# Performance work log

Hardware: AMD Instinct MI355X
Metric: run time of the kernel (lower is better)

Reference implementation:

```python
import jax, jax.numpy as jnp
import numpy as np

B, L, S, H, E = 2, 2048, 2048, 16, 64
EPS = 1e-8


def setup_inputs() -> dict:
    key = jax.random.key(0)
    k1, k2, k3, k4, k5 = jax.random.split(key, 5)
    query = jax.random.normal(k1, (B, L, H, E), dtype=jnp.float32)
    key_t = jax.random.normal(k2, (B, S, H, E), dtype=jnp.float32)
    value = jax.random.normal(k3, (B, S, H, E), dtype=jnp.float32)
    mask_miss_k = jax.random.randint(k4, (B, S, 1), 0, 2).astype(bool)
    mask_miss_q = jax.random.randint(k5, (B, L, 1), 0, 2).astype(bool)
    # monotone per-batch positions -> standard causal structure
    pos = jnp.broadcast_to(jnp.arange(L, dtype=jnp.int32)[None, :, None], (B, L, 1))
    return {"query": query, "key": key_t, "value": value,
            "mask_miss_k": mask_miss_k, "mask_miss_q": mask_miss_q,
            "pos": pos, "causal_mask": 1}


def reference(query, key, value, mask_miss_k, mask_miss_q, pos, causal_mask):
    # query: (B,L,H,E); key/value: (B,S,H,E)
    E_ = query.shape[-1]
    scale = 1.0 / np.sqrt(E_)
    scores = jnp.einsum('blhe,bshe->bhls', query, key)  # (B,H,L,S)
    if causal_mask:
        p = pos[..., 0]  # (B,L)
        causal_add = jnp.where(p[:, None, :] > p[:, :, None],
                               -jnp.inf, 0.0).astype(scores.dtype)  # (B,L,S)
        scores = scores + causal_add[:, None, :, :]
    # additive -inf masks for missing keys / queries
    m_k = jnp.where(mask_miss_k[..., 0][:, None, None, :], -jnp.inf, 0.0).astype(scores.dtype)
    m_q = jnp.where(mask_miss_q[..., 0][:, None, :, None], -jnp.inf, 0.0).astype(scores.dtype)
    # NOTE: scale multiplies (scores + M_k) exactly as in the original
    att = jnp.maximum(jax.nn.softmax(scale * (scores + m_k), axis=-1) + m_q, 0.0)
    # entropy of (post-relu, possibly unnormalized) attention weights
    entropy = -jnp.sum(att * jnp.log(jnp.clip(att, EPS, None)), axis=-1)  # (B,H,L)
    entropy = jnp.nan_to_num(entropy, nan=0.0)
    A = jnp.nan_to_num(att)  # dropout p=0 -> identity, then nan_to_num
    V = jnp.einsum('bhls,bshd->blhd', A, value)  # (B,L,H,E)
    return V, A, entropy
```

## Files before the change

kernel.cpp:

```cpp
#include <hip/hip_runtime.h>

#define BB 2
#define LL 2048
#define SS 2048
#define HH 16
#define EE 64
#define HE (HH*EE)
#define TS 64
#define SCALEF 0.125f
#define NEGBIG (-1e30f)

typedef __bf16 bf8 __attribute__((ext_vector_type(8)));
typedef float f4v __attribute__((ext_vector_type(4)));
typedef unsigned int u32;
typedef unsigned short u16;

#define V_ELEMS  ((size_t)BB*LL*HH*EE)
#define A_BASE   (V_ELEMS)
#define ENT_BASE (A_BASE + (size_t)BB*HH*LL*SS)

__device__ __forceinline__ u16 bfb(float f) {
    u32 u = __builtin_bit_cast(u32, f);
    return (u16)((u + 0x7fffu + ((u >> 16) & 1u)) >> 16);
}
__device__ __forceinline__ int swz8(int r) { return (((r) & 7) ^ (((r) >> 3) & 7)) << 4; }

__device__ __forceinline__ f4v mfma16(bf8 a, bf8 b, f4v c) {
    return __builtin_amdgcn_mfma_f32_16x16x32_bf16(a, b, c, 0, 0, 0);
}
__device__ __forceinline__ int maskv(const void* p, int i, int isB) {
    return isB ? (int)((const unsigned char*)p)[i] : ((const int*)p)[i];
}
__device__ __forceinline__ void barrier_lds() {
    asm volatile("s_waitcnt lgkmcnt(0)" ::: "memory");
    __builtin_amdgcn_s_barrier();
    asm volatile("" ::: "memory");
}
__device__ __forceinline__ uint4 pack8(float4 f0, float4 f1) {
    uint4 wv;
    wv.x = bfb(f0.x) | ((u32)bfb(f0.y) << 16);
    wv.y = bfb(f0.z) | ((u32)bfb(f0.w) << 16);
    wv.z = bfb(f1.x) | ((u32)bfb(f1.y) << 16);
    wv.w = bfb(f1.z) | ((u32)bfb(f1.w) << 16);
    return wv;
}

__device__ __forceinline__ void stage128x64(const float* __restrict__ src,
                                            char* lds, int tid) {
    const int r = tid >> 2, seg = tid & 3;
    const float* rp = src + (size_t)r * HE + seg * 16;
    float4 f0 = *(const float4*)(rp + 0);
    float4 f1 = *(const float4*)(rp + 4);
    float4 f2 = *(const float4*)(rp + 8);
    float4 f3 = *(const float4*)(rp + 12);
    const int base = r * 128 + seg * 32;
    *(uint4*)(void*)(lds + ((base +  0) ^ swz8(r))) = pack8(f0, f1);
    *(uint4*)(void*)(lds + ((base + 16) ^ swz8(r))) = pack8(f2, f3);
}

__global__ __launch_bounds__(512, 4) void k_fused(
    const float* __restrict__ Qg, const float* __restrict__ Kg, const float* __restrict__ Vg,
    const void* __restrict__ mk, const void* __restrict__ mq,
    float* __restrict__ outF)
{
    __shared__ __align__(16) char ldsP[16384];
    __shared__ __align__(16) char ldsK[2][8192];
    __shared__ __align__(16) char ldsVT[2][8192];
    __shared__ float ldsKM[SS];
    __shared__ int sFlag;

    const int blk = blockIdx.x;
    const int xcd = blk & 7, idx = blk >> 3;
    const int bh  = xcd * 4 + (idx & 3);
    const int band = 15 - (idx >> 2);
    const int b = bh >> 4, h = bh & 15;
    const int tid = threadIdx.x;
    const int w = tid >> 6, lane = tid & 63, g = lane >> 4, le = lane & 15;

    int isB;
    {
        const unsigned char* c = (const unsigned char*)mk;
        unsigned acc = 0;
        #pragma unroll
        for (int j = 0; j < 8; ++j) {
            const int off = tid + j * 512;
            if (off & 3) acc |= c[off];
        }
        if (tid == 0) sFlag = 0;
        __syncthreads();
        if (acc) atomicOr(&sFlag, 1);
        __syncthreads();
        isB = sFlag;
    }
    for (int i = tid; i < SS; i += 512)
        ldsKM[i] = maskv(mk, b * SS + i, isB) ? NEGBIG : 0.f;

    const float* Qb = Qg + (size_t)b * LL * HE + h * EE;
    const float* Kb = Kg + (size_t)b * SS * HE + h * EE;
    const float* Vb = Vg + (size_t)b * SS * HE + h * EE;

    const int l0 = band * 128;
    const int lbase = l0 + w * 16 + g * 4;
    const int whi = l0 + w * 16 + 15;
    const int ta  = whi >> 6;
    const int ntile = 2 * (band + 1);

    stage128x64(Qb + (size_t)l0 * HE, ldsP, tid);
    __syncthreads();
    const int qr = w * 16 + le;
    bf8 qf0 = *(const bf8*)(void*)(ldsP + ((qr * 128 +  0 + g * 16) ^ swz8(qr)));
    bf8 qf1 = *(const bf8*)(void*)(ldsP + ((qr * 128 + 64 + g * 16) ^ swz8(qr)));
    barrier_lds();

    const int kr = tid >> 3, ksg = tid & 7;
    const float* kbase = Kb + (size_t)kr * HE + ksg * 8;
    const int koff = (kr * 128 + ksg * 16) ^ swz8(kr);
    const int vrp = tid >> 4, vei = tid & 15;
    const float* vbase = Vb + (size_t)(2 * vrp) * HE + vei * 4;

    float M[4], D[4], T[4];
    #pragma unroll
    for (int r = 0; r < 4; ++r) { M[r] = NEGBIG; D[r] = 0.f; T[r] = 0.f; }

    float4 ka = *(const float4*)(kbase);
    float4 kb2 = *(const float4*)(kbase + 4);
    *(uint4*)(void*)(&ldsK[0][0] + koff) = pack8(ka, kb2);
    if (ntile > 1) {
        const float* kp = kbase + (size_t)TS * HE;
        ka = *(const float4*)(kp); kb2 = *(const float4*)(kp + 4);
    }
    barrier_lds();
    int cur = 0;

    for (int st = 0; st < ntile; ++st) {
        const int s0 = st * TS;
        if (st + 1 < ntile) {
            *(uint4*)(void*)(&ldsK[cur ^ 1][0] + koff) = pack8(ka, kb2);
            if (st + 2 < ntile) {
                const float* kp = kbase + (size_t)(st + 2) * TS * HE;
                ka = *(const float4*)(kp); kb2 = *(const float4*)(kp + 4);
            }
        }
        if (s0 <= whi) {
            f4v acc[4];
            float tm[4] = {NEGBIG, NEGBIG, NEGBIG, NEGBIG};
            #pragma unroll
            for (int cb = 0; cb < 4; ++cb) {
                const int sr = cb * 16 + le;
                bf8 k0 = *(const bf8*)(void*)(&ldsK[cur][0] + ((sr * 128 +  0 + g * 16) ^ swz8(sr)));
                bf8 k1 = *(const bf8*)(void*)(&ldsK[cur][0] + ((sr * 128 + 64 + g * 16) ^ swz8(sr)));
                f4v a = {0.f, 0.f, 0.f, 0.f};
                a = mfma16(qf0, k0, a);
                a = mfma16(qf1, k1, a);
                const float km = ldsKM[s0 + cb * 16 + le];
                const int s = s0 + cb * 16 + le;
                #pragma unroll
                for (int r = 0; r < 4; ++r) {
                    float z = a[r] * SCALEF + km;
                    if (s > lbase + r) z = NEGBIG;
                    acc[cb][r] = z;
                    tm[r] = fmaxf(tm[r], z);
                }
            }
            #pragma unroll
            for (int r = 0; r < 4; ++r) {
                #pragma unroll
                for (int msk = 1; msk < 16; msk <<= 1)
                    tm[r] = fmaxf(tm[r], __shfl_xor(tm[r], msk));
                const float mn  = fmaxf(M[r], tm[r]);
                const float fre = __expf(M[r] - mn);
                float ed = 0.f, et = 0.f;
                #pragma unroll
                for (int cb = 0; cb < 4; ++cb) {
                    const float z = acc[cb][r];
                    const float e = __expf(z - mn);
                    ed += e; et += e * z;
                }
                D[r] = D[r] * fre + ed;
                T[r] = T[r] * fre + et;
                M[r] = mn;
            }
        }
        barrier_lds();
        cur ^= 1;
    }

    float C[4];
    #pragma unroll
    for (int r = 0; r < 4; ++r) {
        #pragma unroll
        for (int msk = 1; msk < 16; msk <<= 1) {
            const float Mo = __shfl_xor(M[r], msk);
            const float Do = __shfl_xor(D[r], msk);
            const float To = __shfl_xor(T[r], msk);
            const float mn = fmaxf(M[r], Mo);
            const float fa = __expf(M[r] - mn);
            const float fb = __expf(Mo  - mn);
            D[r] = D[r] * fa + Do * fb;
            T[r] = T[r] * fa + To * fb;
            M[r] = mn;
        }
        const int l = lbase + r;
        const bool valid = (M[r] > -1e29f) && (maskv(mq, b * LL + l, isB) == 0);
        C[r] = valid ? (M[r] + __logf(D[r])) : 1e30f;
        const float ent = valid ? (C[r] - T[r] / D[r]) : 0.f;
        if (le == 0) outF[ENT_BASE + (size_t)bh * LL + l] = ent;
    }

    float* const Arow0 = outF + A_BASE + ((size_t)bh * LL + l0) * SS;

    {
        const int rr = lane >> 2, cc = lane & 3;
        float* dst0 = Arow0 + (size_t)(w * 16 + rr) * SS;
        const f4v zz = {0.f, 0.f, 0.f, 0.f};
        for (int c = (ta + 1) * TS + cc * 4; c < SS; c += 16)
            *(f4v*)(void*)(dst0 + c) = zz;
    }

    f4v O[4];
    #pragma unroll
    for (int eb = 0; eb < 4; ++eb) O[eb] = (f4v){0.f, 0.f, 0.f, 0.f};

    ka  = *(const float4*)(kbase);
    kb2 = *(const float4*)(kbase + 4);
    float4 va  = *(const float4*)(vbase);
    float4 vb2 = *(const float4*)(vbase + HE);
    *(uint4*)(void*)(&ldsK[0][0] + koff) = pack8(ka, kb2);
    {
        const float* pa_ = &va.x; const float* pb_ = &vb2.x;
        #pragma unroll
        for (int i = 0; i < 4; ++i) {
            const int e = vei * 4 + i;
            const u32 pk = (u32)bfb(pa_[i]) | ((u32)bfb(pb_[i]) << 16);
            *(u32*)(void*)(&ldsVT[0][0] + ((e * 128 + vrp * 4) ^ swz8(e))) = pk;
        }
    }
    if (ntile > 1) {
        const float* kp = kbase + (size_t)TS * HE;
        const float* vp = vbase + (size_t)TS * HE;
        ka = *(const float4*)(kp); kb2 = *(const float4*)(kp + 4);
        va = *(const float4*)(vp); vb2 = *(const float4*)(vp + HE);
    }
    barrier_lds();
    cur = 0;
    char* const myP = ldsP + w * 2048;

    for (int st = 0; st < ntile; ++st) {
        const int s0 = st * TS;
        if (st + 1 < ntile) {
            *(uint4*)(void*)(&ldsK[cur ^ 1][0] + koff) = pack8(ka, kb2);
            {
                const float* pa_ = &va.x; const float* pb_ = &vb2.x;
                #pragma unroll
                for (int i = 0; i < 4; ++i) {
                    const int e = vei * 4 + i;
                    const u32 pk = (u32)bfb(pa_[i]) | ((u32)bfb(pb_[i]) << 16);
                    *(u32*)(void*)(&ldsVT[cur ^ 1][0] + ((e * 128 + vrp * 4) ^ swz8(e))) = pk;
                }
            }
            if (st + 2 < ntile) {
                const float* kp = kbase + (size_t)(st + 2) * TS * HE;
                const float* vp = vbase + (size_t)(st + 2) * TS * HE;
                ka = *(const float4*)(kp); kb2 = *(const float4*)(kp + 4);
                va = *(const float4*)(vp); vb2 = *(const float4*)(vp + HE);
            }
        }
        if (st <= ta) {
            f4v acc[4];
            #pragma unroll
            for (int cb = 0; cb < 4; ++cb) {
                const int sr = cb * 16 + le;
                bf8 k0 = *(const bf8*)(void*)(&ldsK[cur][0] + ((sr * 128 +  0 + g * 16) ^ swz8(sr)));
                bf8 k1 = *(const bf8*)(void*)(&ldsK[cur][0] + ((sr * 128 + 64 + g * 16) ^ swz8(sr)));
                f4v a = {0.f, 0.f, 0.f, 0.f};
                a = mfma16(qf0, k0, a);
                a = mfma16(qf1, k1, a);
                acc[cb] = a;
            }
            #pragma unroll
            for (int cb = 0; cb < 4; ++cb) {
                const float km = ldsKM[s0 + cb * 16 + le];
                const int s = s0 + cb * 16 + le;
                #pragma unroll
                for (int r = 0; r < 4; ++r) {
                    float z = acc[cb][r] * SCALEF + km;
                    if (s > lbase + r) z = NEGBIG;
                    const float p = __expf(z - C[r]);
                    const int row = g * 4 + r;
                    *(u16*)(void*)(myP + ((row * 128 + (cb * 16 + le) * 2) ^ swz8(row))) = bfb(p);
                    outF[A_BASE + ((size_t)bh * LL + (l0 + w * 16 + row)) * SS + s] = p;
                }
            }
            asm volatile("s_waitcnt lgkmcnt(0)" ::: "memory");

            #pragma unroll
            for (int kkb = 0; kkb < 2; ++kkb) {
                bf8 pa = *(const bf8*)(void*)(myP + ((le * 128 + kkb * 64 + g * 16) ^ swz8(le)));
                #pragma unroll
                for (int eb = 0; eb < 4; ++eb) {
                    const int e = eb * 16 + le;
                    bf8 vb = *(const bf8*)(void*)(&ldsVT[cur][0] + ((e * 128 + kkb * 64 + g * 16) ^ swz8(e)));
                    O[eb] = mfma16(pa, vb, O[eb]);
                }
            }
        }
        barrier_lds();
        cur ^= 1;
    }

    #pragma unroll
    for (int eb = 0; eb < 4; ++eb) {
        #pragma unroll
        for (int r = 0; r < 4; ++r) {
            const int l = lbase + r;
            outF[((size_t)(b * LL + l) * HH + h) * EE + eb * 16 + le] = O[eb][r];
        }
    }
}

extern "C" void kernel_launch(void* const* d_in, const int* in_sizes, int n_in,
                              void* d_out, int out_size, void* d_ws, size_t ws_size,
                              hipStream_t stream) {
    const float* Q = (const float*)d_in[0];
    const float* K = (const float*)d_in[1];
    const float* V = (const float*)d_in[2];
    const void* mk = d_in[3];
    const void* mq = d_in[4];
    float* outF = (float*)d_out;

    dim3 blk(512), grid(BB * HH * 16);
    hipLaunchKernelGGL(k_fused, grid, blk, 0, stream, Q, K, V, mk, mq, outF);
}
```

Baseline: 221.9 us.

## Transpose QK MFMA so each lane owns one query row, vectorizing A stores

Swaps the MFMA operand order so the score tile is computed transposed: each lane holds one query row and four consecutive key columns. This makes the online softmax statistics scalar per lane, which cuts cross-lane shuffle reductions and exp work in the merge. It also lets the attention-probability writes to global memory be 16-byte float4 stores and the bf16 P writes to LDS be 8-byte packed stores, instead of scattered scalar stores. The trade-off is per-element key-mask loads from LDS and a different LDS write pattern for P that could introduce bank conflicts.

After: 262.4 us. 1.18x slower.

```diff
diff --git a/kernel.cpp b/kernel.cpp
--- a/kernel.cpp
+++ b/kernel.cpp
@@ -100,7 +100,7 @@
     const float* Vb = Vg + (size_t)b * SS * HE + h * EE;
 
     const int l0 = band * 128;
-    const int lbase = l0 + w * 16 + g * 4;
+    const int lrow = l0 + w * 16 + le;
     const int whi = l0 + w * 16 + 15;
     const int ta  = whi >> 6;
     const int ntile = 2 * (band + 1);
@@ -118,9 +118,7 @@
     const int vrp = tid >> 4, vei = tid & 15;
     const float* vbase = Vb + (size_t)(2 * vrp) * HE + vei * 4;
 
-    float M[4], D[4], T[4];
-    #pragma unroll
-    for (int r = 0; r < 4; ++r) { M[r] = NEGBIG; D[r] = 0.f; T[r] = 0.f; }
+    float M = NEGBIG, D = 0.f, T = 0.f;
 
     float4 ka = *(const float4*)(kbase);
     float4 kb2 = *(const float4*)(kbase + 4);
@@ -143,68 +141,63 @@
         }
         if (s0 <= whi) {
             f4v acc[4];
-            float tm[4] = {NEGBIG, NEGBIG, NEGBIG, NEGBIG};
+            float tm = NEGBIG;
             #pragma unroll
             for (int cb = 0; cb < 4; ++cb) {
                 const int sr = cb * 16 + le;
                 bf8 k0 = *(const bf8*)(void*)(&ldsK[cur][0] + ((sr * 128 +  0 + g * 16) ^ swz8(sr)));
                 bf8 k1 = *(const bf8*)(void*)(&ldsK[cur][0] + ((sr * 128 + 64 + g * 16) ^ swz8(sr)));
                 f4v a = {0.f, 0.f, 0.f, 0.f};
-                a = mfma16(qf0, k0, a);
-                a = mfma16(qf1, k1, a);
-                const float km = ldsKM[s0 + cb * 16 + le];
-                const int s = s0 + cb * 16 + le;
+                a = mfma16(k0, qf0, a);
+                a = mfma16(k1, qf1, a);
                 #pragma unroll
                 for (int r = 0; r < 4; ++r) {
-                    float z = a[r] * SCALEF + km;
-                    if (s > lbase + r) z = NEGBIG;
+                    const int s = s0 + cb * 16 + g * 4 + r;
+                    float z = a[r] * SCALEF + ldsKM[s];
+                    if (s > lrow) z = NEGBIG;
                     acc[cb][r] = z;
-                    tm[r] = fmaxf(tm[r], z);
-                }
-            }
-            #pragma unroll
-            for (int r = 0; r < 4; ++r) {
-                #pragma unroll
-                for (int msk = 1; msk < 16; msk <<= 1)
-                    tm[r] = fmaxf(tm[r], __shfl_xor(tm[r], msk));
-                const float mn  = fmaxf(M[r], tm[r]);
-                const float fre = __expf(M[r] - mn);
-                float ed = 0.f, et = 0.f;
-                #pragma unroll
-                for (int cb = 0; cb < 4; ++cb) {
+                    tm = fmaxf(tm, z);
+                }
+            }
+            tm = fmaxf(tm, __shfl_xor(tm, 16));
+            tm = fmaxf(tm, __shfl_xor(tm, 32));
+            const float mn  = fmaxf(M, tm);
+            const float fre = __expf(M - mn);
+            float ed = 0.f, et = 0.f;
+            #pragma unroll
+            for (int cb = 0; cb < 4; ++cb) {
+                #pragma unroll
+                for (int r = 0; r < 4; ++r) {
                     const float z = acc[cb][r];
                     const float e = __expf(z - mn);
                     ed += e; et += e * z;
                 }
-                D[r] = D[r] * fre + ed;
-                T[r] = T[r] * fre + et;
-                M[r] = mn;
-            }
+            }
+            D = D * fre + ed;
+            T = T * fre + et;
+            M = mn;
         }
         barrier_lds();
         cur ^= 1;
     }
 
-    float C[4];
     #pragma unroll
-    for (int r = 0; r < 4; ++r) {
-        #pragma unroll
-        for (int msk = 1; msk < 16; msk <<= 1) {
-            const float Mo = __shfl_xor(M[r], msk);
-            const float Do = __shfl_xor(D[r], msk);
-            const float To = __shfl_xor(T[r], msk);
-            const float mn = fmaxf(M[r], Mo);
-            const float fa = __expf(M[r] - mn);
-            const float fb = __expf(Mo  - mn);
-            D[r] = D[r] * fa + Do * fb;
-            T[r] = T[r] * fa + To * fb;
-            M[r] = mn;
-        }
-        const int l = lbase + r;
-        const bool valid = (M[r] > -1e29f) && (maskv(mq, b * LL + l, isB) == 0);
-        C[r] = valid ? (M[r] + __logf(D[r])) : 1e30f;
-        const float ent = valid ? (C[r] - T[r] / D[r]) : 0.f;
-        if (le == 0) outF[ENT_BASE + (size_t)bh * LL + l] = ent;
+    for (int msk = 16; msk <= 32; msk <<= 1) {
+        const float Mo = __shfl_xor(M, msk);
+        const float Do = __shfl_xor(D, msk);
+        const float To = __shfl_xor(T, msk);
+        const float mn = fmaxf(M, Mo);
+        const float fa = __expf(M - mn);
+        const float fb = __expf(Mo - mn);
+        D = D * fa + Do * fb;
+        T = T * fa + To * fb;
+        M = mn;
+    }
+    const bool valid = (M > -1e29f) && (maskv(mq, b * LL + lrow, isB) == 0);
+    const float C = valid ? (M + __logf(D)) : 1e30f;
+    if (g == 0) {
+        const float ent = valid ? (C - T / D) : 0.f;
+        outF[ENT_BASE + (size_t)bh * LL + lrow] = ent;
     }
 
     float* const Arow0 = outF + A_BASE + ((size_t)bh * LL + l0) * SS;
@@ -244,6 +237,7 @@
     barrier_lds();
     cur = 0;
     char* const myP = ldsP + w * 2048;
+    float* const myArow = Arow0 + (size_t)(w * 16 + le) * SS;
 
     for (int st = 0; st < ntile; ++st) {
         const int s0 = st * TS;
@@ -273,23 +267,27 @@
                 bf8 k0 = *(const bf8*)(void*)(&ldsK[cur][0] + ((sr * 128 +  0 + g * 16) ^ swz8(sr)));
                 bf8 k1 = *(const bf8*)(void*)(&ldsK[cur][0] + ((sr * 128 + 64 + g * 16) ^ swz8(sr)));
                 f4v a = {0.f, 0.f, 0.f, 0.f};
-                a = mfma16(qf0, k0, a);
-                a = mfma16(qf1, k1, a);
+                a = mfma16(k0, qf0, a);
+                a = mfma16(k1, qf1, a);
                 acc[cb] = a;
             }
             #pragma unroll
             for (int cb = 0; cb < 4; ++cb) {
-                const float km = ldsKM[s0 + cb * 16 + le];
-                const int s = s0 + cb * 16 + le;
+                const int sbase = s0 + cb * 16 + g * 4;
+                float pr[4];
                 #pragma unroll
                 for (int r = 0; r < 4; ++r) {
-                    float z = acc[cb][r] * SCALEF + km;
-                    if (s > lbase + r) z = NEGBIG;
-                    const float p = __expf(z - C[r]);
-                    const int row = g * 4 + r;
-                    *(u16*)(void*)(myP + ((row * 128 + (cb * 16 + le) * 2) ^ swz8(row))) = bfb(p);
-                    outF[A_BASE + ((size_t)bh * LL + (l0 + w * 16 + row)) * SS + s] = p;
-                }
+                    const int s = sbase + r;
+                    float z = acc[cb][r] * SCALEF + ldsKM[s];
+                    if (s > lrow) z = NEGBIG;
+                    pr[r] = __expf(z - C);
+                }
+                const f4v pvv = {pr[0], pr[1], pr[2], pr[3]};
+                *(f4v*)(void*)(myArow + sbase) = pvv;
+                uint2 pk;
+                pk.x = (u32)bfb(pr[0]) | ((u32)bfb(pr[1]) << 16);
+                pk.y = (u32)bfb(pr[2]) | ((u32)bfb(pr[3]) << 16);
+                *(uint2*)(void*)(myP + ((le * 128 + cb * 32 + g * 8) ^ swz8(le))) = pk;
             }
             asm volatile("s_waitcnt lgkmcnt(0)" ::: "memory");
 
@@ -308,6 +306,7 @@
         cur ^= 1;
     }
 
+    const int lbase = l0 + w * 16 + g * 4;
     #pragma unroll
     for (int eb = 0; eb < 4; ++eb) {
         #pragma unroll
```
